# Kernel optimization log

Hardware: AMD Instinct MI355X
Metric: run time of the kernel (lower is better)

The kernel has to match this reference:

```python
import jax, jax.numpy as jnp
import numpy as np

V, D, DFF, L, H, N, K, NB, R = 32000, 512, 2048, 4, 8, 64, 8, 32, 64
B, S = 2, 512
DH = D // H


def _layernorm(x, g, b, eps=1e-5):
    m = x.mean(-1, keepdims=True)
    v = ((x - m) ** 2).mean(-1, keepdims=True)
    return (x - m) * jax.lax.rsqrt(v + eps) * g + b


def _forward(input_ids, token_emb, pos_emb, basis_A, basis_emb, recipe,
             Wq, bq, Wk, bk, Wv, bv, Ws, bs, Wup, bup, Wdown, bdown,
             ln1_g, ln1_b, ln2_g, ln2_b, alpha, lnf_g, lnf_b):
    Bc, Sc = input_ids.shape
    x = token_emb[input_ids] + pos_emb[:Sc][None]          # [B,S,D]
    causal = jnp.tril(jnp.ones((Sc, Sc), dtype=bool))
    neg = jnp.asarray(-jnp.inf, x.dtype)
    scale = jnp.asarray(1.0 / np.sqrt(DH), x.dtype)
    for i in range(L):
        rec = recipe[i]                                    # [N,NB]
        neuron_emb = jax.nn.softmax(rec, -1) @ basis_emb   # [N,D] routing embedding
        # ---- SimpleRouter on norm1(x) ----
        n1 = _layernorm(x, ln1_g[i], ln1_b[i])
        q = (n1 @ Wq[i] + bq[i]).reshape(Bc, Sc, H, DH)
        k = (n1 @ Wk[i] + bk[i]).reshape(Bc, Sc, H, DH)
        v = (n1 @ Wv[i] + bv[i]).reshape(Bc, Sc, H, DH)
        attn = jnp.einsum('bqhd,bkhd->bhqk', q, k) * scale
        attn = jnp.where(causal[None, None], attn, neg)
        attn = jax.nn.softmax(attn, -1)
        ctx = jnp.einsum('bhqk,bkhd->bqhd', attn, v).reshape(Bc, Sc, D)
        query = jnp.concatenate([n1, ctx], -1) @ Ws[i] + bs[i]   # [B,S,D]
        scores = query @ neuron_emb.T                            # [B,S,N]
        topk_scores, topk_idx = jax.lax.top_k(scores, K)
        weights = jax.nn.softmax(topk_scores, -1)                # [B,S,K]
        # ---- BasisResidualFFN on norm2(x) ----
        n2 = _layernorm(x, ln2_g[i], ln2_b[i])
        sel = jax.nn.softmax(rec[topk_idx], -1)                  # [B,S,K,NB]
        token_recipe = (sel * weights[..., None]).sum(2)         # [B,S,NB]
        # delta = x @ W_A @ W_A^T with W_A = token_recipe . basis_A, computed
        # WITHOUT materializing [B,S,D,R] (same math, associativity only)
        proj = jnp.einsum('bsd,ndr->bsnr', n2, basis_A)          # [B,S,NB,R]
        h = jnp.einsum('bsn,bsnr->bsr', token_recipe, proj)      # [B,S,R]
        delta = jnp.einsum('bsn,bsr,ndr->bsd', token_recipe, h, basis_A)
        xf = n2 + alpha[i] * delta
        ff = jax.nn.gelu(xf @ Wup[i] + bup[i], approximate=False) @ Wdown[i] + bdown[i]
        x = x + ff                                               # dropout=0 (eval)
    x = _layernorm(x, lnf_g, lnf_b)
    return x @ token_emb.T                                       # tied head


def setup_inputs() -> dict:
    key = jax.random.key(0)
    ks = iter(jax.random.split(key, 40))
    std = 0.02
    nrm = lambda shape, s=std: jax.random.normal(next(ks), shape, jnp.float32) * s
    input_ids = jax.random.randint(next(ks), (B, S), 0, V)
    basis_A = jax.random.normal(next(ks), (NB, D, R), jnp.float32)
    basis_A = basis_A / jnp.linalg.norm(basis_A.reshape(NB, -1), axis=-1)[:, None, None]
    basis_emb = jax.random.normal(next(ks), (NB, D), jnp.float32)
    basis_emb = basis_emb / jnp.linalg.norm(basis_emb, axis=-1, keepdims=True)
    return dict(
        input_ids=input_ids,
        token_emb=nrm((V, D)), pos_emb=nrm((S, D)),
        basis_A=basis_A, basis_emb=basis_emb,
        recipe=jax.random.normal(next(ks), (L, N, NB), jnp.float32) * 0.5,
        Wq=nrm((L, D, D)), bq=jnp.zeros((L, D)),
        Wk=nrm((L, D, D)), bk=jnp.zeros((L, D)),
        Wv=nrm((L, D, D)), bv=jnp.zeros((L, D)),
        Ws=nrm((L, 2 * D, D)), bs=jnp.zeros((L, D)),
        Wup=nrm((L, D, DFF)), bup=jnp.zeros((L, DFF)),
        Wdown=nrm((L, DFF, D)), bdown=jnp.zeros((L, D)),
        ln1_g=jnp.ones((L, D)), ln1_b=jnp.zeros((L, D)),
        ln2_g=jnp.ones((L, D)), ln2_b=jnp.zeros((L, D)),
        alpha=jnp.full((L,), 0.1, jnp.float32),
        lnf_g=jnp.ones((D,)), lnf_b=jnp.zeros((D,)),
    )


def reference(input_ids, token_emb, pos_emb, basis_A, basis_emb, recipe,
              Wq, bq, Wk, bk, Wv, bv, Ws, bs, Wup, bup, Wdown, bdown,
              ln1_g, ln1_b, ln2_g, ln2_b, alpha, lnf_g, lnf_b):
    return _forward(input_ids, token_emb, pos_emb, basis_A, basis_emb, recipe,
                    Wq, bq, Wk, bk, Wv, bv, Ws, bs, Wup, bup, Wdown, bdown,
                    ln1_g, ln1_b, ln2_g, ln2_b, alpha, lnf_g, lnf_b)
```

## Files before the change

kernel.cpp:

```cpp
#include <hip/hip_runtime.h>
#include <hip/hip_bf16.h>
#include <math.h>

#define V_  32000
#define D_  512
#define DFF_ 2048
#define L_  4
#define H_  8
#define N_  64
#define K_  8
#define NB_ 32
#define R_  64
#define B_  2
#define S_  512
#define T_  1024
#define DH_ 64

typedef short bhalf8 __attribute__((ext_vector_type(8)));
typedef float floatx4 __attribute__((ext_vector_type(4)));

#define GLOAD16(gp, lp) __builtin_amdgcn_global_load_lds( \
    (const __attribute__((address_space(1))) void*)(gp), \
    (__attribute__((address_space(3))) void*)(lp), 16, 0, 0)

__device__ __forceinline__ float gelu_f(float v) {
    return 0.5f * v * (1.0f + erff(v * 0.70710678118654752f));
}

__device__ __forceinline__ unsigned pk2(float a, float b) {
    unsigned ua = (unsigned)__bfloat16_as_ushort(__float2bfloat16(a));
    unsigned ub = (unsigned)__bfloat16_as_ushort(__float2bfloat16(b));
    return ua | (ub << 16);
}

template<int BM, int BN, int WR, int WC, int EPI, bool SWAP = false, int SWZ = 0>
__global__ __launch_bounds__(256) void gemm_mfma(
    const __hip_bfloat16* __restrict__ A, int lda, long sA,
    const __hip_bfloat16* __restrict__ Bt, int ldb, long sB,
    const float* __restrict__ bias,
    const float* __restrict__ aux,
    void* __restrict__ Cv, int ldc, long sC,
    int Kdim)
{
    constexpr int FM = BM / WR / 16;
    constexpr int FN = BN / WC / 16;
    constexpr int ACH = BM * 8;
    constexpr int BCH = BN * 8;
    __shared__ __align__(16) short As[2][BM * 64];
    __shared__ __align__(16) short Bs[2][BN * 64];
    const int tid = threadIdx.x;
    const int z = blockIdx.z;
    A  += (long)z * sA;
    Bt += (long)z * sB;
    int bm, bn;
    if constexpr (SWZ == 1) {
        constexpr int MT = T_ / BM;
        constexpr int NP = V_ / BN;
        constexpr int PPX = (NP + 7) / 8;
        int d = blockIdx.x;
        int xcd = d & 7, k = d >> 3;
        int ty = xcd * PPX + (k >> 3);
        if (ty >= NP) return;
        bm = (k & (MT - 1)) * BM;
        bn = ty * BN;
    } else {
        bm = (SWAP ? blockIdx.x : blockIdx.y) * BM;
        bn = (SWAP ? blockIdx.y : blockIdx.x) * BN;
    }
    const int w = tid >> 6, lane = tid & 63;
    const int wr = w / WC, wc = w % WC;
    const int moff = wr * (BM / WR), noff = wc * (BN / WC);
    floatx4 acc[FM][FN] = {};

    auto stage = [&](int buf, int k0) {
        #pragma unroll
        for (int i = 0; i < ACH / 256; i++) {
            int c = tid + i * 256;
            int m = c >> 3, u = (c & 7) ^ (m & 7);
            const __hip_bfloat16* src = A + (long)(bm + m) * lda + k0 + u * 8;
            char* dst = (char*)&As[buf][0] + (w * 64 + i * 256) * 16;
            GLOAD16(src, dst);
        }
        #pragma unroll
        for (int i = 0; i < BCH / 256; i++) {
            int c = tid + i * 256;
            int m = c >> 3, u = (c & 7) ^ (m & 7);
            const __hip_bfloat16* src = Bt + (long)(bn + m) * ldb + k0 + u * 8;
            char* dst = (char*)&Bs[buf][0] + (w * 64 + i * 256) * 16;
            GLOAD16(src, dst);
        }
    };

    const int nt = Kdim >> 6;
    stage(0, 0);
    __syncthreads();
    int cur = 0;
    for (int t = 0; t < nt; ++t) {
        if (t + 1 < nt) stage(cur ^ 1, (t + 1) * 64);
        #pragma unroll
        for (int kk = 0; kk < 2; kk++) {
            bhalf8 af[FM], bf[FN];
            #pragma unroll
            for (int fm = 0; fm < FM; fm++) {
                int row = moff + fm * 16 + (lane & 15);
                int u = (kk * 4 + (lane >> 4)) ^ (row & 7);
                af[fm] = *(const bhalf8*)((const char*)&As[cur][0] + row * 128 + u * 16);
            }
            #pragma unroll
            for (int fn = 0; fn < FN; fn++) {
                int row = noff + fn * 16 + (lane & 15);
                int u = (kk * 4 + (lane >> 4)) ^ (row & 7);
                bf[fn] = *(const bhalf8*)((const char*)&Bs[cur][0] + row * 128 + u * 16);
            }
            #pragma unroll
            for (int fm = 0; fm < FM; fm++)
                #pragma unroll
                for (int fn = 0; fn < FN; fn++)
                    acc[fm][fn] = __builtin_amdgcn_mfma_f32_16x16x32_bf16(
                        af[fm], bf[fn], acc[fm][fn], 0, 0, 0);
        }
        __syncthreads();
        cur ^= 1;
    }

    float* Cf = (float*)Cv;
    __hip_bfloat16* Cb = (__hip_bfloat16*)Cv;
    __hip_bfloat16* vtb = (EPI == 5) ? (__hip_bfloat16*)(void*)aux : nullptr;
    const long zoff = (long)z * sC;
    const int lr = lane >> 4, lc = lane & 15;
    float alphaV = (EPI == 3) ? bias[0] : 0.f;
    #pragma unroll
    for (int fm = 0; fm < FM; fm++) {
        #pragma unroll
        for (int fn = 0; fn < FN; fn++) {
            int cN = bn + noff + fn * 16 + lc;
            float bv = (EPI == 3 || !bias || (EPI == 6 && z != 0)) ? 0.f : bias[cN];
            #pragma unroll
            for (int i = 0; i < 4; i++) {
                int rM = bm + moff + fm * 16 + lr * 4 + i;
                long idx = zoff + (long)rM * ldc + cN;
                float v = acc[fm][fn][i] + bv;
                if constexpr (EPI == 0) Cf[idx] = v;
                else if constexpr (EPI == 1) Cb[idx] = __float2bfloat16(v);
                else if constexpr (EPI == 2) Cb[idx] = __float2bfloat16(gelu_f(v));
                else if constexpr (EPI == 3)
                    Cb[idx] = __float2bfloat16(aux[idx] + alphaV * acc[fm][fn][i]);
                else if constexpr (EPI == 4) Cf[idx] += v;
                else if constexpr (EPI == 5) {
                    __hip_bfloat16 bvv = __float2bfloat16(v);
                    Cb[idx] = bvv;
                    if (cN >= 1024) {
                        int hh = (cN - 1024) >> 6, dh = (cN - 1024) & 63;
                        int bb = rM >> 9, ss = rM & 511;
                        vtb[(((long)bb * 8 + hh) * 64 + dh) * 512 + ss] = bvv;
                    }
                }
                else if constexpr (EPI == 6) atomicAdd(&Cf[idx], v);
            }
        }
    }
}

__global__ __launch_bounds__(256) void attn_mfma(
    const __hip_bfloat16* __restrict__ qkv,
    const __hip_bfloat16* __restrict__ vt,
    __hip_bfloat16* __restrict__ catB)
{
    __shared__ short pbuf[4][16][72];
    const int tid = threadIdx.x;
    const int w = tid >> 6, lane = tid & 63;
    const int g = lane >> 4, ql = lane & 15;
    const int h = blockIdx.y, b = blockIdx.z;
    const int qbase = blockIdx.x * 64 + w * 16;

    const long qrow = ((long)(b * S_ + qbase + ql)) * 1536 + h * DH_;
    bhalf8 qa0 = *(const bhalf8*)(qkv + qrow + g * 8);
    bhalf8 qa1 = *(const bhalf8*)(qkv + qrow + 32 + g * 8);
    const __hip_bfloat16* kB = qkv + 512;
    const __hip_bfloat16* vbase = vt + ((long)(b * H_ + h)) * DH_ * S_;

    floatx4 o[4] = {};
    float m = -INFINITY, ls = 0.f;
    const float SC = 0.125f * 1.44269504088896f;
    const int nblk = blockIdx.x + 1;

    for (int kvb = 0; kvb < nblk; kvb++) {
        const int kb0 = kvb * 64;
        floatx4 st[4];
        #pragma unroll
        for (int t = 0; t < 4; t++) {
            long krow = ((long)(b * S_ + kb0 + t * 16 + ql)) * 1536 + h * DH_;
            bhalf8 ka0 = *(const bhalf8*)(kB + krow + g * 8);
            bhalf8 ka1 = *(const bhalf8*)(kB + krow + 32 + g * 8);
            floatx4 z = {};
            z = __builtin_amdgcn_mfma_f32_16x16x32_bf16(ka0, qa0, z, 0, 0, 0);
            z = __builtin_amdgcn_mfma_f32_16x16x32_bf16(ka1, qa1, z, 0, 0, 0);
            st[t] = z;
        }
        const int q = qbase + ql;
        float p[4][4];
        float m4 = -INFINITY;
        #pragma unroll
        for (int t = 0; t < 4; t++)
            #pragma unroll
            for (int i = 0; i < 4; i++) {
                int kv = kb0 + t * 16 + g * 4 + i;
                float v = (kv <= q) ? st[t][i] * SC : -INFINITY;
                p[t][i] = v; m4 = fmaxf(m4, v);
            }
        m4 = fmaxf(m4, __shfl_xor(m4, 16));
        m4 = fmaxf(m4, __shfl_xor(m4, 32));
        float mnew = fmaxf(m, m4);
        float corr = exp2f(m - mnew);
        m = mnew;
        float lsum = 0.f;
        #pragma unroll
        for (int t = 0; t < 4; t++)
            #pragma unroll
            for (int i = 0; i < 4; i++) {
                float e = exp2f(p[t][i] - mnew);
                p[t][i] = e; lsum += e;
            }
        lsum += __shfl_xor(lsum, 16);
        lsum += __shfl_xor(lsum, 32);
        ls = ls * corr + lsum;
        unsigned* prow = (unsigned*)&pbuf[w][ql][0];
        #pragma unroll
        for (int t = 0; t < 4; t++) {
            prow[t * 8 + g * 2]     = pk2(p[t][0], p[t][1]);
            prow[t * 8 + g * 2 + 1] = pk2(p[t][2], p[t][3]);
        }
        #pragma unroll
        for (int i = 0; i < 4; i++) {
            float c = __shfl(corr, g * 4 + i);
            #pragma unroll
            for (int dt = 0; dt < 4; dt++) o[dt][i] *= c;
        }
        __syncthreads();
        #pragma unroll
        for (int ks = 0; ks < 2; ks++) {
            bhalf8 pa = *(const bhalf8*)&pbuf[w][ql][ks * 32 + g * 8];
            #pragma unroll
            for (int dt = 0; dt < 4; dt++) {
                bhalf8 vb = *(const bhalf8*)(vbase + (long)(dt * 16 + ql) * S_ + kb0 + ks * 32 + g * 8);
                o[dt] = __builtin_amdgcn_mfma_f32_16x16x32_bf16(pa, vb, o[dt], 0, 0, 0);
            }
        }
        __syncthreads();
    }
    const float inv = 1.f / ls;
    #pragma unroll
    for (int i = 0; i < 4; i++) {
        float iv = __shfl(inv, g * 4 + i);
        int trow = b * S_ + qbase + g * 4 + i;
        #pragma unroll
        for (int dt = 0; dt < 4; dt++)
            catB[(long)trow * 1024 + 512 + h * DH_ + dt * 16 + ql] =
                __float2bfloat16(o[dt][i] * iv);
    }
}

__device__ __forceinline__ void tcvt_dev(const float* in, int ldn, long sIn,
                                         __hip_bfloat16* out, int ldk, long sOut,
                                         int bx, int by, int bz, float (*tsh)[33]) {
    in  += (long)bz * sIn;
    out += (long)bz * sOut;
    int k0 = by * 32, n0 = bx * 32;
    int tx = threadIdx.x & 31, ty = threadIdx.x >> 5;
    #pragma unroll
    for (int r = 0; r < 4; r++) tsh[ty * 4 + r][tx] = in[(long)(k0 + ty * 4 + r) * ldn + n0 + tx];
    __syncthreads();
    #pragma unroll
    for (int r = 0; r < 4; r++)
        out[(long)(n0 + ty * 4 + r) * ldk + k0 + tx] = __float2bfloat16(tsh[tx][ty * 4 + r]);
}

__global__ __launch_bounds__(256) void prologue_kernel(
    const float* __restrict__ temb, __hip_bfloat16* __restrict__ tembB,
    const float* __restrict__ basisA, __hip_bfloat16* __restrict__ projT,
    __hip_bfloat16* __restrict__ deltaT,
    const float* __restrict__ bq, const float* __restrict__ bk,
    const float* __restrict__ bv, float* __restrict__ bqkv,
    const float* __restrict__ Wq, const float* __restrict__ Wk,
    const float* __restrict__ Wv, __hip_bfloat16* __restrict__ qkvT,
    const float* __restrict__ Wup, __hip_bfloat16* __restrict__ WupT,
    const float* __restrict__ Wdn, __hip_bfloat16* __restrict__ WdnT,
    const float* __restrict__ Ws, __hip_bfloat16* __restrict__ WsB,
    const int* __restrict__ ids, const float* __restrict__ pemb,
    float* __restrict__ x)
{
    __shared__ float tsh[32][33];
    const int blk = blockIdx.x, tid = threadIdx.x;
    if (blk < 16000) {
        long i = ((long)blk * 256 + tid) * 4;
        float4 v = *(const float4*)(temb + i);
        tembB[i]     = __float2bfloat16(v.x);
        tembB[i + 1] = __float2bfloat16(v.y);
        tembB[i + 2] = __float2bfloat16(v.z);
        tembB[i + 3] = __float2bfloat16(v.w);
    } else if (blk < 20096) {
        long i = (long)(blk - 16000) * 256 + tid;
        int r = i & 63; int d = (i >> 6) & 511; int n = i >> 15;
        __hip_bfloat16 v = __float2bfloat16(basisA[i]);
        projT[((long)n * R_ + r) * D_ + d] = v;
        deltaT[(long)d * (NB_ * R_) + n * R_ + r] = v;
    } else if (blk < 20120) {
        int i = (blk - 20096) * 256 + tid;
        int l = i / 1536, j = i % 1536;
        float v = (j < 512) ? bq[l * 512 + j] : (j < 1024) ? bk[l * 512 + j - 512]
                                                           : bv[l * 512 + j - 1024];
        bqkv[i] = v;
    } else if (blk < 21144) {
        int lin = blk - 20120;
        tcvt_dev(Wq, D_, (long)D_ * D_, qkvT, D_, (long)1536 * D_,
                 lin & 15, (lin >> 4) & 15, lin >> 8, tsh);
    } else if (blk < 22168) {
        int lin = blk - 21144;
        tcvt_dev(Wk, D_, (long)D_ * D_, qkvT + 512 * 512, D_, (long)1536 * D_,
                 lin & 15, (lin >> 4) & 15, lin >> 8, tsh);
    } else if (blk < 23192) {
        int lin = blk - 22168;
        tcvt_dev(Wv, D_, (long)D_ * D_, qkvT + 1024 * 512, D_, (long)1536 * D_,
                 lin & 15, (lin >> 4) & 15, lin >> 8, tsh);
    } else if (blk < 27288) {
        int lin = blk - 23192;
        tcvt_dev(Wup, DFF_, (long)D_ * DFF_, WupT, D_, (long)D_ * DFF_,
                 lin & 63, (lin >> 6) & 15, lin >> 10, tsh);
    } else if (blk < 31384) {
        int lin = blk - 27288;
        tcvt_dev(Wdn, D_, (long)DFF_ * D_, WdnT, DFF_, (long)DFF_ * D_,
                 lin & 15, (lin >> 4) & 63, lin >> 10, tsh);
    } else if (blk < 33432) {
        long i = ((long)(blk - 31384) * 256 + tid) * 4;
        float4 v = *(const float4*)(Ws + i);
        WsB[i]     = __float2bfloat16(v.x);
        WsB[i + 1] = __float2bfloat16(v.y);
        WsB[i + 2] = __float2bfloat16(v.z);
        WsB[i + 3] = __float2bfloat16(v.w);
    } else {
        int t = blk - 33432;
        int s = t % S_;
        int id = ids[t];
        for (int d = tid; d < D_; d += 256)
            x[(long)t * D_ + d] = temb[(long)id * D_ + d] + pemb[(long)s * D_ + d];
    }
}

__device__ __forceinline__ void ln_dev(const float* row, const float* g, const float* b,
                                       float* outf, __hip_bfloat16* outb, int ldo,
                                       long t, float* red) {
    int tid = threadIdx.x;
    float v0 = row[tid], v1 = row[tid + 256];
    red[tid] = v0 + v1; __syncthreads();
    for (int off = 128; off; off >>= 1) { if (tid < off) red[tid] += red[tid + off]; __syncthreads(); }
    float mean = red[0] * (1.0f / D_); __syncthreads();
    float d0 = v0 - mean, d1 = v1 - mean;
    red[tid] = d0 * d0 + d1 * d1; __syncthreads();
    for (int off = 128; off; off >>= 1) { if (tid < off) red[tid] += red[tid + off]; __syncthreads(); }
    float rstd = rsqrtf(red[0] * (1.0f / D_) + 1e-5f);
    float o0 = d0 * rstd * g[tid]       + b[tid];
    float o1 = d1 * rstd * g[tid + 256] + b[tid + 256];
    if (outf) {
        outf[t * D_ + tid]       = o0;
        outf[t * D_ + tid + 256] = o1;
    }
    outb[t * ldo + tid]       = __float2bfloat16(o0);
    outb[t * ldo + tid + 256] = __float2bfloat16(o1);
}

__global__ __launch_bounds__(256) void prep_kernel(
    const float* __restrict__ x,
    const float* __restrict__ ln1g, const float* __restrict__ ln1b,
    const float* __restrict__ ln2g, const float* __restrict__ ln2b,
    const float* __restrict__ rec, const float* __restrict__ bemb,
    const float* __restrict__ bs,
    __hip_bfloat16* __restrict__ catB, float* __restrict__ buf1,
    __hip_bfloat16* __restrict__ n2B,
    __hip_bfloat16* __restrict__ neb, float* __restrict__ sel,
    float* __restrict__ bsne)
{
    __shared__ float red[256];
    int blk = blockIdx.x, tid = threadIdx.x;
    if (blk < 1024) {
        ln_dev(x + (long)blk * D_, ln1g, ln1b, nullptr, catB, 1024, blk, red);
    } else if (blk < 2048) {
        long t = blk - 1024;
        ln_dev(x + t * D_, ln2g, ln2b, buf1, n2B, 512, t, red);
    } else {
        int n = blk - 2048;
        __shared__ float wsm[NB_];
        if (tid == 0) {
            float mx = -1e30f;
            for (int i = 0; i < NB_; i++) mx = fmaxf(mx, rec[n * NB_ + i]);
            float sm = 0.f;
            for (int i = 0; i < NB_; i++) { float e = expf(rec[n * NB_ + i] - mx); wsm[i] = e; sm += e; }
            float inv = 1.f / sm;
            for (int i = 0; i < NB_; i++) wsm[i] *= inv;
        }
        __syncthreads();
        if (tid < NB_) sel[n * NB_ + tid] = wsm[tid];
        float part = 0.f;
        for (int d = tid; d < D_; d += 256) {
            float acc = 0.f;
            #pragma unroll
            for (int nb = 0; nb < NB_; nb++) acc += wsm[nb] * bemb[nb * D_ + d];
            neb[(long)n * D_ + d] = __float2bfloat16(acc);
            part += bs[d] * acc;
        }
        red[tid] = part; __syncthreads();
        for (int off = 128; off; off >>= 1) { if (tid < off) red[tid] += red[tid + off]; __syncthreads(); }
        if (tid == 0) bsne[n] = red[0];
    }
}

__global__ __launch_bounds__(256) void ln_kernel(const float* __restrict__ in,
                                                 const float* __restrict__ g,
                                                 const float* __restrict__ b,
                                                 __hip_bfloat16* __restrict__ outb) {
    __shared__ float red[256];
    long t = blockIdx.x;
    ln_dev(in + t * D_, g, b, nullptr, outb, 512, t, red);
}

__global__ __launch_bounds__(256) void route_hg(
    const float* __restrict__ scb, const float* __restrict__ sel,
    const float* __restrict__ P, __hip_bfloat16* __restrict__ g)
{
    int t = blockIdx.x, tid = threadIdx.x;
    __shared__ float trl[32];
    __shared__ float hl[64];
    if (tid < 64) {
        int lane = tid;
        float myval = scb[(long)t * N_ + lane];
        float topv[K_]; int topi[K_];
        #pragma unroll
        for (int kk = 0; kk < K_; kk++) {
            float v = myval; int idx = lane;
            #pragma unroll
            for (int off = 32; off; off >>= 1) {
                float ov = __shfl_down(v, off);
                int oi = __shfl_down(idx, off);
                if (ov > v || (ov == v && oi < idx)) { v = ov; idx = oi; }
            }
            v = __shfl(v, 0); idx = __shfl(idx, 0);
            topv[kk] = v; topi[kk] = idx;
            if (lane == idx) myval = -INFINITY;
        }
        float mx = topv[0];
        float w[K_], sum = 0.f;
        #pragma unroll
        for (int kk = 0; kk < K_; kk++) { w[kk] = expf(topv[kk] - mx); sum += w[kk]; }
        float inv = 1.f / sum;
        if (lane < NB_) {
            float a = 0.f;
            #pragma unroll
            for (int kk = 0; kk < K_; kk++) a += w[kk] * inv * sel[topi[kk] * NB_ + lane];
            trl[lane] = a;
        }
    }
    __syncthreads();
    if (tid < 64) {
        float acc = 0.f;
        const float* p = P + (long)t * 2048 + tid;
        #pragma unroll
        for (int n = 0; n < 32; n++) acc += trl[n] * p[n * 64];
        hl[tid] = acc;
    }
    __syncthreads();
    #pragma unroll
    for (int j = 0; j < 8; j++) {
        int idx = tid * 8 + j;
        int n = idx >> 6, r = idx & 63;
        g[(long)t * 2048 + idx] = __float2bfloat16(trl[n] * hl[r]);
    }
}

extern "C" void kernel_launch(void* const* d_in, const int* in_sizes, int n_in,
                              void* d_out, int out_size, void* d_ws, size_t ws_size,
                              hipStream_t stream) {
    const int*   ids    = (const int*)d_in[0];
    const float* temb   = (const float*)d_in[1];
    const float* pemb   = (const float*)d_in[2];
    const float* basisA = (const float*)d_in[3];
    const float* bemb   = (const float*)d_in[4];
    const float* recipe = (const float*)d_in[5];
    const float* Wq = (const float*)d_in[6],  *bq = (const float*)d_in[7];
    const float* Wk = (const float*)d_in[8],  *bk = (const float*)d_in[9];
    const float* Wv = (const float*)d_in[10], *bv = (const float*)d_in[11];
    const float* Ws = (const float*)d_in[12], *bs = (const float*)d_in[13];
    const float* Wup = (const float*)d_in[14], *bup = (const float*)d_in[15];
    const float* Wdn = (const float*)d_in[16], *bdn = (const float*)d_in[17];
    const float* ln1g = (const float*)d_in[18], *ln1b = (const float*)d_in[19];
    const float* ln2g = (const float*)d_in[20], *ln2b = (const float*)d_in[21];
    const float* alpha = (const float*)d_in[22];
    const float* lnfg = (const float*)d_in[23], *lnfb = (const float*)d_in[24];
    float* out = (float*)d_out;
    float* W = (float*)d_ws;

    float* x    = W + 0;
    float* buf1 = W + 524288;
    float* scb  = W + 1048576;
    float* bsne = W + 1114112;
    float* sel  = W + 1212416;
    float* P    = W + 1214464;
    float* bqkv = W + 3835904;
    __hip_bfloat16* SB = (__hip_bfloat16*)(W + 3844096);
    __hip_bfloat16* tembB  = SB + 0;
    __hip_bfloat16* qkvT   = SB + 16384000;
    __hip_bfloat16* WsB    = SB + 19529728;
    __hip_bfloat16* WupT   = SB + 21626880;
    __hip_bfloat16* WdnT   = SB + 25821184;
    __hip_bfloat16* projT  = SB + 30015488;
    __hip_bfloat16* deltaT = SB + 31064064;
    __hip_bfloat16* neB    = SB + 32112640;
    __hip_bfloat16* catB   = SB + 32145408;
    __hip_bfloat16* WsneT  = SB + 33193984;
    __hip_bfloat16* n2B    = SB + 33718272;
    __hip_bfloat16* xfB    = SB + 34242560;
    __hip_bfloat16* gB     = SB + 34766848;
    __hip_bfloat16* ffhB   = SB + 36864000;
    __hip_bfloat16* qkvB   = SB + 38961152;
    __hip_bfloat16* VtB    = SB + 40534016;

    dim3 blk(256);
    prologue_kernel<<<34456, blk, 0, stream>>>(
        temb, tembB, basisA, projT, deltaT, bq, bk, bv, bqkv,
        Wq, Wk, Wv, qkvT, Wup, WupT, Wdn, WdnT, Ws, WsB, ids, pemb, x);

    for (int l = 0; l < L_; l++) {
        prep_kernel<<<2112, blk, 0, stream>>>(
            x, ln1g + l * D_, ln1b + l * D_, ln2g + l * D_, ln2b + l * D_,
            recipe + (long)l * N_ * NB_, bemb, bs + l * D_,
            catB, buf1, n2B, neB, sel, bsne);
        gemm_mfma<64, 64, 2, 2, 5><<<dim3(24, 16), blk, 0, stream>>>(
            catB, 1024, 0, qkvT + (long)l * 1536 * 512, D_, 0, bqkv + l * 1536,
            (const float*)VtB, qkvB, 1536, 0, D_);
        gemm_mfma<64, 64, 2, 2, 1><<<dim3(16, 1), blk, 0, stream>>>(
            neB, D_, 0, WsB + (long)l * 1024 * 512, D_, 0, nullptr, nullptr,
            WsneT, 1024, 0, D_);
        attn_mfma<<<dim3(8, H_, B_), blk, 0, stream>>>(qkvB, VtB, catB);
        gemm_mfma<128, 64, 2, 2, 0><<<dim3(1, 8), blk, 0, stream>>>(
            catB, 1024, 0, WsneT, 1024, 0, bsne, nullptr, scb, N_, 0, 1024);
        gemm_mfma<128, 64, 2, 2, 0><<<dim3(1, 8, NB_), blk, 0, stream>>>(
            n2B, D_, 0, projT, D_, (long)R_ * D_, nullptr, nullptr, P, NB_ * R_, R_, D_);
        route_hg<<<T_, blk, 0, stream>>>(scb, sel, P, gB);
        gemm_mfma<64, 64, 2, 2, 3><<<dim3(8, 16), blk, 0, stream>>>(
            gB, NB_ * R_, 0, deltaT, NB_ * R_, 0, alpha + l, buf1,
            xfB, D_, 0, NB_ * R_);
        gemm_mfma<64, 64, 2, 2, 2><<<dim3(32, 16), blk, 0, stream>>>(
            xfB, D_, 0, WupT + (long)l * D_ * DFF_, D_, 0, bup + l * DFF_, nullptr,
            ffhB, DFF_, 0, D_);
        gemm_mfma<64, 64, 2, 2, 6><<<dim3(8, 16, 2), blk, 0, stream>>>(
            ffhB, DFF_, 1024, WdnT + (long)l * DFF_ * D_, DFF_, 1024, bdn + l * D_, nullptr,
            x, D_, 0, 1024);
    }
    ln_kernel<<<T_, blk, 0, stream>>>(x, lnfg, lnfb, n2B);
    gemm_mfma<128, 64, 2, 2, 0, false, 1><<<dim3(4032), blk, 0, stream>>>(
        n2B, D_, 0, tembB, D_, 0, nullptr, nullptr, out, V_, 0, D_);
}
```

Measured before the change: 592.5 us.

## Merge per-layer GEMMs into one launch and fuse routing scores into route kernel

Refactors the GEMM body into a device function so one mega_gemm launch can run the QKV projection, the Ws·neuron-embedding product (now stored transposed as a K-major matrix) and the basis projection GEMM as separate block ranges. The routing score GEMM is removed and recomputed inside route_hg as a per-token dot product over catB, dropping a launch and the scb buffer. LayerNorm now uses one wave per row with shuffle reductions and vectorized loads and stores, replacing block-level shared-memory reductions. Per layer this cuts kernel launches and small under-filled GEMMs, at the cost of scalar FMA score work in route_hg and uneven block shapes in the merged launch.

```diff
diff --git a/kernel.cpp b/kernel.cpp
--- a/kernel.cpp
+++ b/kernel.cpp
@@ -33,61 +33,43 @@
     return ua | (ub << 16);
 }
 
-template<int BM, int BN, int WR, int WC, int EPI, bool SWAP = false, int SWZ = 0>
-__global__ __launch_bounds__(256) void gemm_mfma(
+template<int BM, int BN, int WR, int WC, int EPI>
+__device__ __forceinline__ void gemm_dev(
+    short* __restrict__ lds,
     const __hip_bfloat16* __restrict__ A, int lda, long sA,
     const __hip_bfloat16* __restrict__ Bt, int ldb, long sB,
     const float* __restrict__ bias,
     const float* __restrict__ aux,
     void* __restrict__ Cv, int ldc, long sC,
-    int Kdim)
+    int Kdim, int bm, int bn, int z)
 {
     constexpr int FM = BM / WR / 16;
     constexpr int FN = BN / WC / 16;
     constexpr int ACH = BM * 8;
     constexpr int BCH = BN * 8;
-    __shared__ __align__(16) short As[2][BM * 64];
-    __shared__ __align__(16) short Bs[2][BN * 64];
-    const int tid = threadIdx.x;
-    const int z = blockIdx.z;
+    constexpr int HALF = (BM + BN) * 64;
     A  += (long)z * sA;
     Bt += (long)z * sB;
-    int bm, bn;
-    if constexpr (SWZ == 1) {
-        constexpr int MT = T_ / BM;
-        constexpr int NP = V_ / BN;
-        constexpr int PPX = (NP + 7) / 8;
-        int d = blockIdx.x;
-        int xcd = d & 7, k = d >> 3;
-        int ty = xcd * PPX + (k >> 3);
-        if (ty >= NP) return;
-        bm = (k & (MT - 1)) * BM;
-        bn = ty * BN;
-    } else {
-        bm = (SWAP ? blockIdx.x : blockIdx.y) * BM;
-        bn = (SWAP ? blockIdx.y : blockIdx.x) * BN;
-    }
+    const int tid = threadIdx.x;
     const int w = tid >> 6, lane = tid & 63;
     const int wr = w / WC, wc = w % WC;
     const int moff = wr * (BM / WR), noff = wc * (BN / WC);
     floatx4 acc[FM][FN] = {};
 
     auto stage = [&](int buf, int k0) {
+        char* baseA = (char*)(lds + buf * HALF);
+        char* baseB = (char*)(lds + buf * HALF + BM * 64);
         #pragma unroll
         for (int i = 0; i < ACH / 256; i++) {
             int c = tid + i * 256;
             int m = c >> 3, u = (c & 7) ^ (m & 7);
-            const __hip_bfloat16* src = A + (long)(bm + m) * lda + k0 + u * 8;
-            char* dst = (char*)&As[buf][0] + (w * 64 + i * 256) * 16;
-            GLOAD16(src, dst);
+            GLOAD16(A + (long)(bm + m) * lda + k0 + u * 8, baseA + (w * 64 + i * 256) * 16);
         }
         #pragma unroll
         for (int i = 0; i < BCH / 256; i++) {
             int c = tid + i * 256;
             int m = c >> 3, u = (c & 7) ^ (m & 7);
-            const __hip_bfloat16* src = Bt + (long)(bn + m) * ldb + k0 + u * 8;
-            char* dst = (char*)&Bs[buf][0] + (w * 64 + i * 256) * 16;
-            GLOAD16(src, dst);
+            GLOAD16(Bt + (long)(bn + m) * ldb + k0 + u * 8, baseB + (w * 64 + i * 256) * 16);
         }
     };
 
@@ -97,6 +79,8 @@
     int cur = 0;
     for (int t = 0; t < nt; ++t) {
         if (t + 1 < nt) stage(cur ^ 1, (t + 1) * 64);
+        const char* baseA = (const char*)(lds + cur * HALF);
+        const char* baseB = (const char*)(lds + cur * HALF + BM * 64);
         #pragma unroll
         for (int kk = 0; kk < 2; kk++) {
             bhalf8 af[FM], bf[FN];
@@ -104,13 +88,13 @@
             for (int fm = 0; fm < FM; fm++) {
                 int row = moff + fm * 16 + (lane & 15);
                 int u = (kk * 4 + (lane >> 4)) ^ (row & 7);
-                af[fm] = *(const bhalf8*)((const char*)&As[cur][0] + row * 128 + u * 16);
+                af[fm] = *(const bhalf8*)(baseA + row * 128 + u * 16);
             }
             #pragma unroll
             for (int fn = 0; fn < FN; fn++) {
                 int row = noff + fn * 16 + (lane & 15);
                 int u = (kk * 4 + (lane >> 4)) ^ (row & 7);
-                bf[fn] = *(const bhalf8*)((const char*)&Bs[cur][0] + row * 128 + u * 16);
+                bf[fn] = *(const bhalf8*)(baseB + row * 128 + u * 16);
             }
             #pragma unroll
             for (int fm = 0; fm < FM; fm++)
@@ -158,6 +142,61 @@
                 else if constexpr (EPI == 6) atomicAdd(&Cf[idx], v);
             }
         }
+    }
+}
+
+template<int BM, int BN, int WR, int WC, int EPI, int SWZ = 0>
+__global__ __launch_bounds__(256) void gemm_mfma(
+    const __hip_bfloat16* __restrict__ A, int lda, long sA,
+    const __hip_bfloat16* __restrict__ Bt, int ldb, long sB,
+    const float* __restrict__ bias,
+    const float* __restrict__ aux,
+    void* __restrict__ Cv, int ldc, long sC,
+    int Kdim)
+{
+    __shared__ short lds[2 * (BM + BN) * 64];
+    int bm, bn;
+    if constexpr (SWZ == 1) {
+        constexpr int MT = T_ / BM;
+        constexpr int NP = V_ / BN;
+        constexpr int PPX = (NP + 7) / 8;
+        int d = blockIdx.x;
+        int xcd = d & 7, k = d >> 3;
+        int ty = xcd * PPX + (k >> 3);
+        if (ty >= NP) return;
+        bm = (k & (MT - 1)) * BM;
+        bn = ty * BN;
+    } else {
+        bm = blockIdx.y * BM;
+        bn = blockIdx.x * BN;
+    }
+    gemm_dev<BM, BN, WR, WC, EPI>(lds, A, lda, sA, Bt, ldb, sB, bias, aux,
+                                  Cv, ldc, sC, Kdim, bm, bn, blockIdx.z);
+}
+
+__global__ __launch_bounds__(256) void mega_gemm(
+    const __hip_bfloat16* __restrict__ catB, const __hip_bfloat16* __restrict__ qkvT,
+    const float* __restrict__ bqkv, __hip_bfloat16* __restrict__ VtB,
+    __hip_bfloat16* __restrict__ qkvB,
+    const __hip_bfloat16* __restrict__ WsB, const __hip_bfloat16* __restrict__ neB,
+    __hip_bfloat16* __restrict__ WsneK,
+    const __hip_bfloat16* __restrict__ n2B, const __hip_bfloat16* __restrict__ projT,
+    float* __restrict__ P)
+{
+    __shared__ short lds[2 * 192 * 64];
+    int blk = blockIdx.x;
+    if (blk < 384) {
+        gemm_dev<64, 64, 2, 2, 5>(lds, catB, 1024, 0, qkvT, D_, 0, bqkv,
+                                  (const float*)VtB, qkvB, 1536, 0, D_,
+                                  (blk / 24) * 64, (blk % 24) * 64, 0);
+    } else if (blk < 400) {
+        gemm_dev<64, 64, 2, 2, 1>(lds, WsB, D_, 0, neB, D_, 0, nullptr, nullptr,
+                                  WsneK, N_, 0, D_, (blk - 384) * 64, 0, 0);
+    } else {
+        int local = blk - 400;
+        gemm_dev<128, 64, 2, 2, 0>(lds, n2B, D_, 0, projT, D_, (long)R_ * D_,
+                                   nullptr, nullptr, P, NB_ * R_, R_, D_,
+                                   (local & 7) * 128, 0, local >> 3);
     }
 }
 
@@ -346,26 +385,43 @@
     }
 }
 
-__device__ __forceinline__ void ln_dev(const float* row, const float* g, const float* b,
-                                       float* outf, __hip_bfloat16* outb, int ldo,
-                                       long t, float* red) {
-    int tid = threadIdx.x;
-    float v0 = row[tid], v1 = row[tid + 256];
-    red[tid] = v0 + v1; __syncthreads();
-    for (int off = 128; off; off >>= 1) { if (tid < off) red[tid] += red[tid + off]; __syncthreads(); }
-    float mean = red[0] * (1.0f / D_); __syncthreads();
-    float d0 = v0 - mean, d1 = v1 - mean;
-    red[tid] = d0 * d0 + d1 * d1; __syncthreads();
-    for (int off = 128; off; off >>= 1) { if (tid < off) red[tid] += red[tid + off]; __syncthreads(); }
-    float rstd = rsqrtf(red[0] * (1.0f / D_) + 1e-5f);
-    float o0 = d0 * rstd * g[tid]       + b[tid];
-    float o1 = d1 * rstd * g[tid + 256] + b[tid + 256];
+__device__ __forceinline__ float wave_sum(float v) {
+    #pragma unroll
+    for (int off = 1; off < 64; off <<= 1) v += __shfl_xor(v, off);
+    return v;
+}
+
+__device__ __forceinline__ void ln_wave(const float* __restrict__ row,
+                                        const float* __restrict__ g,
+                                        const float* __restrict__ b,
+                                        float* __restrict__ outf,
+                                        __hip_bfloat16* __restrict__ outb,
+                                        int ldo, long t) {
+    int lane = threadIdx.x & 63;
+    float4 a0 = *(const float4*)(row + lane * 8);
+    float4 a1 = *(const float4*)(row + lane * 8 + 4);
+    float v[8] = {a0.x, a0.y, a0.z, a0.w, a1.x, a1.y, a1.z, a1.w};
+    float s = 0.f;
+    #pragma unroll
+    for (int j = 0; j < 8; j++) s += v[j];
+    float mean = wave_sum(s) * (1.0f / D_);
+    float vs = 0.f;
+    #pragma unroll
+    for (int j = 0; j < 8; j++) { v[j] -= mean; vs += v[j] * v[j]; }
+    float rstd = rsqrtf(wave_sum(vs) * (1.0f / D_) + 1e-5f);
+    float4 g0 = *(const float4*)(g + lane * 8), g1 = *(const float4*)(g + lane * 8 + 4);
+    float4 b0 = *(const float4*)(b + lane * 8), b1 = *(const float4*)(b + lane * 8 + 4);
+    float gg[8] = {g0.x, g0.y, g0.z, g0.w, g1.x, g1.y, g1.z, g1.w};
+    float bb[8] = {b0.x, b0.y, b0.z, b0.w, b1.x, b1.y, b1.z, b1.w};
+    float o[8];
+    #pragma unroll
+    for (int j = 0; j < 8; j++) o[j] = v[j] * rstd * gg[j] + bb[j];
     if (outf) {
-        outf[t * D_ + tid]       = o0;
-        outf[t * D_ + tid + 256] = o1;
-    }
-    outb[t * ldo + tid]       = __float2bfloat16(o0);
-    outb[t * ldo + tid + 256] = __float2bfloat16(o1);
+        *(float4*)(outf + t * D_ + lane * 8)     = make_float4(o[0], o[1], o[2], o[3]);
+        *(float4*)(outf + t * D_ + lane * 8 + 4) = make_float4(o[4], o[5], o[6], o[7]);
+    }
+    uint4 pkv = make_uint4(pk2(o[0], o[1]), pk2(o[2], o[3]), pk2(o[4], o[5]), pk2(o[6], o[7]));
+    *(uint4*)(outb + (long)t * ldo + lane * 8) = pkv;
 }
 
 __global__ __launch_bounds__(256) void prep_kernel(
@@ -379,16 +435,17 @@
     __hip_bfloat16* __restrict__ neb, float* __restrict__ sel,
     float* __restrict__ bsne)
 {
-    __shared__ float red[256];
-    int blk = blockIdx.x, tid = threadIdx.x;
-    if (blk < 1024) {
-        ln_dev(x + (long)blk * D_, ln1g, ln1b, nullptr, catB, 1024, blk, red);
-    } else if (blk < 2048) {
-        long t = blk - 1024;
-        ln_dev(x + t * D_, ln2g, ln2b, buf1, n2B, 512, t, red);
+    int blk = blockIdx.x, tid = threadIdx.x, w = tid >> 6;
+    if (blk < 256) {
+        long t = blk * 4 + w;
+        ln_wave(x + t * D_, ln1g, ln1b, nullptr, catB, 1024, t);
+    } else if (blk < 512) {
+        long t = (blk - 256) * 4 + w;
+        ln_wave(x + t * D_, ln2g, ln2b, buf1, n2B, 512, t);
     } else {
-        int n = blk - 2048;
+        __shared__ float red[256];
         __shared__ float wsm[NB_];
+        int n = blk - 512;
         if (tid == 0) {
             float mx = -1e30f;
             for (int i = 0; i < NB_; i++) mx = fmaxf(mx, rec[n * NB_ + i]);
@@ -417,21 +474,46 @@
                                                  const float* __restrict__ g,
                                                  const float* __restrict__ b,
                                                  __hip_bfloat16* __restrict__ outb) {
-    __shared__ float red[256];
-    long t = blockIdx.x;
-    ln_dev(in + t * D_, g, b, nullptr, outb, 512, t, red);
+    long t = blockIdx.x * 4 + (threadIdx.x >> 6);
+    ln_wave(in + t * D_, g, b, nullptr, outb, 512, t);
 }
 
 __global__ __launch_bounds__(256) void route_hg(
-    const float* __restrict__ scb, const float* __restrict__ sel,
+    const __hip_bfloat16* __restrict__ catB, const __hip_bfloat16* __restrict__ WsneK,
+    const float* __restrict__ bsne, const float* __restrict__ sel,
     const float* __restrict__ P, __hip_bfloat16* __restrict__ g)
 {
     int t = blockIdx.x, tid = threadIdx.x;
+    __shared__ float catf[1024];
+    __shared__ float part[4][64];
     __shared__ float trl[32];
     __shared__ float hl[64];
+    {
+        short4 vv = *(const short4*)(catB + (long)t * 1024 + tid * 4);
+        catf[tid * 4 + 0] = __bfloat162float(*(__hip_bfloat16*)&vv.x);
+        catf[tid * 4 + 1] = __bfloat162float(*(__hip_bfloat16*)&vv.y);
+        catf[tid * 4 + 2] = __bfloat162float(*(__hip_bfloat16*)&vv.z);
+        catf[tid * 4 + 3] = __bfloat162float(*(__hip_bfloat16*)&vv.w);
+    }
+    __syncthreads();
+    int n = tid & 63, q = tid >> 6;
+    {
+        const __hip_bfloat16* wp = WsneK + (long)q * 256 * 64 + n;
+        const float* cf = catf + q * 256;
+        float a0 = 0.f, a1 = 0.f, a2 = 0.f, a3 = 0.f;
+        #pragma unroll 16
+        for (int j = 0; j < 256; j += 4) {
+            a0 = fmaf(cf[j],     __bfloat162float(wp[(j)     * 64]), a0);
+            a1 = fmaf(cf[j + 1], __bfloat162float(wp[(j + 1) * 64]), a1);
+            a2 = fmaf(cf[j + 2], __bfloat162float(wp[(j + 2) * 64]), a2);
+            a3 = fmaf(cf[j + 3], __bfloat162float(wp[(j + 3) * 64]), a3);
+        }
+        part[q][n] = (a0 + a1) + (a2 + a3);
+    }
+    __syncthreads();
     if (tid < 64) {
         int lane = tid;
-        float myval = scb[(long)t * N_ + lane];
+        float myval = part[0][lane] + part[1][lane] + part[2][lane] + part[3][lane] + bsne[lane];
         float topv[K_]; int topi[K_];
         #pragma unroll
         for (int kk = 0; kk < K_; kk++) {
@@ -447,14 +529,14 @@
             if (lane == idx) myval = -INFINITY;
         }
         float mx = topv[0];
-        float w[K_], sum = 0.f;
-        #pragma unroll
-        for (int kk = 0; kk < K_; kk++) { w[kk] = expf(topv[kk] - mx); sum += w[kk]; }
+        float wgt[K_], sum = 0.f;
+        #pragma unroll
+        for (int kk = 0; kk < K_; kk++) { wgt[kk] = expf(topv[kk] - mx); sum += wgt[kk]; }
         float inv = 1.f / sum;
         if (lane < NB_) {
             float a = 0.f;
             #pragma unroll
-            for (int kk = 0; kk < K_; kk++) a += w[kk] * inv * sel[topi[kk] * NB_ + lane];
+            for (int kk = 0; kk < K_; kk++) a += wgt[kk] * inv * sel[topi[kk] * NB_ + lane];
             trl[lane] = a;
         }
     }
@@ -463,15 +545,15 @@
         float acc = 0.f;
         const float* p = P + (long)t * 2048 + tid;
         #pragma unroll
-        for (int n = 0; n < 32; n++) acc += trl[n] * p[n * 64];
+        for (int nn = 0; nn < 32; nn++) acc += trl[nn] * p[nn * 64];
         hl[tid] = acc;
     }
     __syncthreads();
     #pragma unroll
     for (int j = 0; j < 8; j++) {
         int idx = tid * 8 + j;
-        int n = idx >> 6, r = idx & 63;
-        g[(long)t * 2048 + idx] = __float2bfloat16(trl[n] * hl[r]);
+        int nn = idx >> 6, r = idx & 63;
+        g[(long)t * 2048 + idx] = __float2bfloat16(trl[nn] * hl[r]);
     }
 }
 
@@ -499,7 +581,6 @@
 
     float* x    = W + 0;
     float* buf1 = W + 524288;
-    float* scb  = W + 1048576;
     float* bsne = W + 1114112;
     float* sel  = W + 1212416;
     float* P    = W + 1214464;
@@ -514,7 +595,7 @@
     __hip_bfloat16* deltaT = SB + 31064064;
     __hip_bfloat16* neB    = SB + 32112640;
     __hip_bfloat16* catB   = SB + 32145408;
-    __hip_bfloat16* WsneT  = SB + 33193984;
+    __hip_bfloat16* WsneK  = SB + 33193984;
     __hip_bfloat16* n2B    = SB + 33718272;
     __hip_bfloat16* xfB    = SB + 34242560;
     __hip_bfloat16* gB     = SB + 34766848;
@@ -528,22 +609,15 @@
         Wq, Wk, Wv, qkvT, Wup, WupT, Wdn, WdnT, Ws, WsB, ids, pemb, x);
 
     for (int l = 0; l < L_; l++) {
-        prep_kernel<<<2112, blk, 0, stream>>>(
+        prep_kernel<<<576, blk, 0, stream>>>(
             x, ln1g + l * D_, ln1b + l * D_, ln2g + l * D_, ln2b + l * D_,
             recipe + (long)l * N_ * NB_, bemb, bs + l * D_,
             catB, buf1, n2B, neB, sel, bsne);
-        gemm_mfma<64, 64, 2, 2, 5><<<dim3(24, 16), blk, 0, stream>>>(
-            catB, 1024, 0, qkvT + (long)l * 1536 * 512, D_, 0, bqkv + l * 1536,
-            (const float*)VtB, qkvB, 1536, 0, D_);
-        gemm_mfma<64, 64, 2, 2, 1><<<dim3(16, 1), blk, 0, stream>>>(
-            neB, D_, 0, WsB + (long)l * 1024 * 512, D_, 0, nullptr, nullptr,
-            WsneT, 1024, 0, D_);
+        mega_gemm<<<656, blk, 0, stream>>>(
+            catB, qkvT + (long)l * 1536 * 512, bqkv + l * 1536, VtB, qkvB,
+            WsB + (long)l * 1024 * 512, neB, WsneK, n2B, projT, P);
         attn_mfma<<<dim3(8, H_, B_), blk, 0, stream>>>(qkvB, VtB, catB);
-        gemm_mfma<128, 64, 2, 2, 0><<<dim3(1, 8), blk, 0, stream>>>(
-            catB, 1024, 0, WsneT, 1024, 0, bsne, nullptr, scb, N_, 0, 1024);
-        gemm_mfma<128, 64, 2, 2, 0><<<dim3(1, 8, NB_), blk, 0, stream>>>(
-            n2B, D_, 0, projT, D_, (long)R_ * D_, nullptr, nullptr, P, NB_ * R_, R_, D_);
-        route_hg<<<T_, blk, 0, stream>>>(scb, sel, P, gB);
+        route_hg<<<T_, blk, 0, stream>>>(catB, WsneK, bsne, sel, P, gB);
         gemm_mfma<64, 64, 2, 2, 3><<<dim3(8, 16), blk, 0, stream>>>(
             gB, NB_ * R_, 0, deltaT, NB_ * R_, 0, alpha + l, buf1,
             xfB, D_, 0, NB_ * R_);
@@ -554,7 +628,7 @@
             ffhB, DFF_, 1024, WdnT + (long)l * DFF_ * D_, DFF_, 1024, bdn + l * D_, nullptr,
             x, D_, 0, 1024);
     }
-    ln_kernel<<<T_, blk, 0, stream>>>(x, lnfg, lnfb, n2B);
-    gemm_mfma<128, 64, 2, 2, 0, false, 1><<<dim3(4032), blk, 0, stream>>>(
+    ln_kernel<<<256, blk, 0, stream>>>(x, lnfg, lnfb, n2B);
+    gemm_mfma<128, 64, 2, 2, 0, 1><<<dim3(4032), blk, 0, stream>>>(
         n2B, D_, 0, tembB, D_, 0, nullptr, nullptr, out, V_, 0, D_);
 }
```

New measurement: 536.9 us. -9.4%, faster.
